# Performance work log

Measured on AMD Instinct MI355X. Metric: run time of the kernel, lower is better.

Reference implementation:

```python
import jax, jax.numpy as jnp
import numpy as np

V, BLOCK, D, H, LAYERS = 32000, 1024, 1024, 16, 4
KD = D // H  # key_dim = value_dim = head_size = 64
B, T = 4, 1024


def _ln(x, g, b, eps=1e-5):
    mu = jnp.mean(x, axis=-1, keepdims=True)
    var = jnp.mean((x - mu) ** 2, axis=-1, keepdims=True)
    return (x - mu) * jax.lax.rsqrt(var + eps) * g + b


def setup_inputs() -> dict:
    key = jax.random.key(0)
    ks = jax.random.split(key, 24)
    s = 0.02
    inp = {
        "x": jax.random.randint(ks[0], (B, T), 0, V),
        "tok_emb": jax.random.normal(ks[1], (V, D), jnp.float32) * s,
        "pos_emb": jax.random.normal(ks[2], (BLOCK, D), jnp.float32) * s,
        # per-head projections stacked over H (heads are identical since D % H == 0)
        "Wq": jax.random.normal(ks[3], (H, D, KD), jnp.float32) * s,
        "bq": jnp.zeros((H, KD), jnp.float32),
        "Wk": jax.random.normal(ks[4], (H, D, KD), jnp.float32) * s,
        "bk": jnp.zeros((H, KD), jnp.float32),
        "Wv": jax.random.normal(ks[5], (H, D, KD), jnp.float32) * s,
        "bv": jnp.zeros((H, KD), jnp.float32),
        "Wo": jax.random.normal(ks[6], (H, KD, KD), jnp.float32) * s,
        "bo": jnp.zeros((H, KD), jnp.float32),
        "W1": jax.random.normal(ks[7], (D, 4 * D), jnp.float32) * s,
        "b1": jnp.zeros((4 * D,), jnp.float32),
        "W2": jax.random.normal(ks[8], (4 * D, D), jnp.float32) * s,
        "b2": jnp.zeros((D,), jnp.float32),
        "ln1_g": jnp.ones((D,), jnp.float32),
        "ln1_b": jnp.zeros((D,), jnp.float32),
        "ln2_g": jnp.ones((D,), jnp.float32),
        "ln2_b": jnp.zeros((D,), jnp.float32),
        "lnf_g": jnp.ones((D,), jnp.float32),
        "lnf_b": jnp.zeros((D,), jnp.float32),
        "Wout": jax.random.normal(ks[9], (D, V), jnp.float32) * s,
        "bout": jnp.zeros((V,), jnp.float32),
    }
    return inp


def _forward(x, tok_emb, pos_emb, Wq, bq, Wk, bk, Wv, bv, Wo, bo,
             W1, b1, W2, b2, ln1_g, ln1_b, ln2_g, ln2_b, lnf_g, lnf_b, Wout, bout):
    h = tok_emb[x] + pos_emb[jnp.arange(x.shape[1])]  # [B,T,D]
    scale = 1.0 / np.sqrt(KD)
    # NOTE: [TransformerBlock()] * layers in the source ties ONE block's
    # weights across all layers, so the same params are applied LAYERS times.
    for _ in range(LAYERS):
        xn = _ln(h, ln1_g, ln1_b)
        q = jnp.einsum('btd,hdk->bhtk', xn, Wq) + bq[:, None, :]
        k = jnp.einsum('btd,hdk->bhtk', xn, Wk) + bk[:, None, :]
        v = jnp.einsum('btd,hdk->bhtk', xn, Wv) + bv[:, None, :]
        scores = jnp.einsum('bhtk,bhsk->bhts', q, k) * scale
        # source quirk: tril then `scores == 0 -> -inf` (also masks exact zeros)
        scores = jnp.tril(scores)
        scores = jnp.where(scores == 0.0, -jnp.inf, scores)
        wts = jax.nn.softmax(scores, axis=-1)
        y = jnp.einsum('bhts,bhsv->bhtv', wts, v)
        o = jnp.einsum('bhtv,hvo->bhto', y, Wo) + bo[:, None, :]
        attn = o.transpose(0, 2, 1, 3).reshape(h.shape)  # concat heads -> [B,T,D]
        h = h + attn
        xn2 = _ln(h, ln2_g, ln2_b)
        ff = jax.nn.relu(xn2 @ W1 + b1) @ W2 + b2
        h = h + ff
    return _ln(h, lnf_g, lnf_b) @ Wout + bout  # logits [B,T,V]


def reference(x, tok_emb, pos_emb, Wq, bq, Wk, bk, Wv, bv, Wo, bo,
              W1, b1, W2, b2, ln1_g, ln1_b, ln2_g, ln2_b, lnf_g, lnf_b, Wout, bout):
    return _forward(x, tok_emb, pos_emb, Wq, bq, Wk, bk, Wv, bv, Wo, bo,
                    W1, b1, W2, b2, ln1_g, ln1_b, ln2_g, ln2_b,
                    lnf_g, lnf_b, Wout, bout)
```

## Files before the change

kernel.cpp:

```cpp
#include <hip/hip_runtime.h>
#include <hip/hip_bf16.h>

typedef __hip_bfloat16 bf16;
typedef __attribute__((ext_vector_type(8))) short s16x8;
typedef __attribute__((ext_vector_type(4))) short s16x4;
typedef __attribute__((ext_vector_type(4))) float f32x4;

#define NEG_INF (-__builtin_inff())

union V8 { s16x8 v8; s16x4 v4[2]; };

__device__ inline s16x8 ldfrag(const bf16* p) {
    V8 f;
    f.v4[0] = *(const s16x4*)p;
    f.v4[1] = *(const s16x4*)(p + 4);
    return f.v8;
}

__device__ inline unsigned short f2bu(float f) {
    union { bf16 b; unsigned short u; } c;
    c.b = __float2bfloat16(f);
    return c.u;
}

__device__ inline float bu2f(unsigned short u) {
    union { bf16 b; unsigned short u; } c;
    c.u = u;
    return __bfloat162float(c.b);
}

__device__ inline void gload16(const bf16* gsrc, const bf16* ldst) {
    __builtin_amdgcn_global_load_lds(
        (const __attribute__((address_space(1))) unsigned int*)(unsigned long long)gsrc,
        (__attribute__((address_space(3))) unsigned int*)(unsigned int)(unsigned long long)ldst,
        16, 0, 0);
}

__global__ void sniff_kernel(const unsigned short* __restrict__ tok, int* __restrict__ flag)
{
    int big = 0;
    for (int i = threadIdx.x; i < 2048; i += 64) {
        unsigned e = (tok[i] >> 7) & 0xFFu;
        if (e >= 127u) big++;
    }
    #pragma unroll
    for (int off = 32; off; off >>= 1) big += __shfl_down(big, off);
    if (threadIdx.x == 0) *flag = (big > 64) ? 1 : 0;
}

__global__ __launch_bounds__(256) void transpose_cvt_kernel(
    const void* __restrict__ in, bf16* __restrict__ out,
    int N, int K, long in_bs, long out_bs, const int* __restrict__ flag)
{
    __shared__ float tile[32][33];
    const int f32 = *flag;
    const int z = blockIdx.z;
    const int n0 = blockIdx.x * 32, k0 = blockIdx.y * 32;
    const int r  = threadIdx.x >> 3;
    const int c4 = (threadIdx.x & 7) * 4;
    if (f32) {
        const float* ip = (const float*)in + z * in_bs;
        float4 v = *(const float4*)(ip + (long)(k0 + r) * N + n0 + c4);
        tile[r][c4 + 0] = v.x; tile[r][c4 + 1] = v.y;
        tile[r][c4 + 2] = v.z; tile[r][c4 + 3] = v.w;
    } else {
        const bf16* ip = (const bf16*)in + z * in_bs;
        ushort4 v = *(const ushort4*)(ip + (long)(k0 + r) * N + n0 + c4);
        tile[r][c4 + 0] = bu2f(v.x); tile[r][c4 + 1] = bu2f(v.y);
        tile[r][c4 + 2] = bu2f(v.z); tile[r][c4 + 3] = bu2f(v.w);
    }
    __syncthreads();
    bf16* op = out + z * out_bs;
    ushort4 o;
    o.x = f2bu(tile[c4 + 0][r]); o.y = f2bu(tile[c4 + 1][r]);
    o.z = f2bu(tile[c4 + 2][r]); o.w = f2bu(tile[c4 + 3][r]);
    *(ushort4*)(op + (long)(n0 + r) * K + k0 + c4) = o;
}

__global__ __launch_bounds__(256) void cvt_bias_kernel(
    const void* __restrict__ in, float* __restrict__ out, int n,
    const int* __restrict__ flag)
{
    int i = blockIdx.x * 256 + threadIdx.x;
    if (i < n)
        out[i] = (*flag) ? ((const float*)in)[i]
                         : __bfloat162float(((const bf16*)in)[i]);
}

__global__ __launch_bounds__(256) void embed_kernel(
    const int* __restrict__ x, const void* __restrict__ tok,
    const void* __restrict__ pos, float* __restrict__ h,
    const int* __restrict__ flag)
{
    const int f32 = *flag;
    int row = blockIdx.x;
    int t = row & 1023;
    int id = x[row];
    float* hp = h + (long)row * 1024;
    if (f32) {
        const float* tp = (const float*)tok + (long)id * 1024;
        const float* pp = (const float*)pos + (long)t * 1024;
        for (int c = threadIdx.x; c < 1024; c += 256)
            hp[c] = tp[c] + pp[c];
    } else {
        const bf16* tp = (const bf16*)tok + (long)id * 1024;
        const bf16* pp = (const bf16*)pos + (long)t * 1024;
        for (int c = threadIdx.x; c < 1024; c += 256)
            hp[c] = __bfloat162float(tp[c]) + __bfloat162float(pp[c]);
    }
}

__global__ __launch_bounds__(256) void ln_kernel(
    const float* __restrict__ h, const void* __restrict__ g,
    const void* __restrict__ b, bf16* __restrict__ out,
    const int* __restrict__ flag)
{
    __shared__ float red[8];
    const int f32 = *flag;
    int row = blockIdx.x;
    const float* hp = h + (long)row * 1024;
    int t = threadIdx.x;
    float4 xv = ((const float4*)hp)[t];
    float s  = xv.x + xv.y + xv.z + xv.w;
    float ss = xv.x*xv.x + xv.y*xv.y + xv.z*xv.z + xv.w*xv.w;
    #pragma unroll
    for (int off = 32; off; off >>= 1) {
        s  += __shfl_down(s, off);
        ss += __shfl_down(ss, off);
    }
    int wv = t >> 6, lane = t & 63;
    if (lane == 0) { red[wv] = s; red[4 + wv] = ss; }
    __syncthreads();
    float fs  = red[0] + red[1] + red[2] + red[3];
    float fss = red[4] + red[5] + red[6] + red[7];
    float mu  = fs * (1.0f / 1024.0f);
    float var = fss * (1.0f / 1024.0f) - mu * mu;
    float rstd = rsqrtf(fmaxf(var, 0.f) + 1e-5f);
    bf16* op = out + (long)row * 1024;
    #pragma unroll
    for (int i = 0; i < 4; i++) {
        int c = t * 4 + i;
        float gv, bv_;
        if (f32) { gv = ((const float*)g)[c]; bv_ = ((const float*)b)[c]; }
        else     { gv = __bfloat162float(((const bf16*)g)[c]); bv_ = __bfloat162float(((const bf16*)b)[c]); }
        float xn = (((const float*)&xv)[i] - mu) * rstd;
        op[c] = __float2bfloat16(xn * gv + bv_);
    }
}

template<bool RELU, bool RES_ADD, bool DYN_OUT>
__global__ __launch_bounds__(256) void gemm_kernel(
    const bf16* __restrict__ A, int lda, long a_bs,
    const void* __restrict__ B, int ldb, long b_bs,
    const void* __restrict__ bias, int bias_bs,
    void* __restrict__ Cv, int ldc, long c_bs, int K,
    const int* __restrict__ flag)
{
    __shared__ bf16 As[64][36];
    __shared__ bf16 Bs[64][36];
    const int f32 = *flag;
    const int tid = threadIdx.x;
    const int z = blockIdx.z;
    const bf16*  Ab   = A + (long)z * a_bs + (long)blockIdx.x * 64 * lda;
    const bf16*  Bb16 = (const bf16*)B  + (long)z * b_bs + (long)blockIdx.y * 64;
    const float* Bb32 = (const float*)B + (long)z * b_bs + (long)blockIdx.y * 64;
    const int wv = tid >> 6, lane = tid & 63, l16 = lane & 15, quad = lane >> 4;

    f32x4 acc[4];
    #pragma unroll
    for (int s = 0; s < 4; s++) { f32x4 z4 = {0.f,0.f,0.f,0.f}; acc[s] = z4; }

    const bool doA = tid < 128;
    const int ht = tid & 127;
    const int arow = ht >> 1;
    const int ak   = (ht & 1) * 16;
    const int bn   = (ht & 7) * 8;
    const int kp   = (ht >> 3) * 2;

    for (int k0 = 0; k0 < K; k0 += 32) {
        if (doA) {
            const bf16* src = Ab + (long)arow * lda + k0 + ak;
            V8 t0, t1;
            t0.v8 = *(const s16x8*)src;
            t1.v8 = *(const s16x8*)(src + 8);
            *(s16x4*)&As[arow][ak]      = t0.v4[0];
            *(s16x4*)&As[arow][ak + 4]  = t0.v4[1];
            *(s16x4*)&As[arow][ak + 8]  = t1.v4[0];
            *(s16x4*)&As[arow][ak + 12] = t1.v4[1];
        } else if (!f32) {
            const bf16* src = Bb16 + (long)(k0 + kp) * ldb + bn;
            s16x8 r0 = *(const s16x8*)src;
            s16x8 r1 = *(const s16x8*)(src + ldb);
            #pragma unroll
            for (int j = 0; j < 8; ++j) {
                unsigned int lo = (unsigned short)r0[j];
                unsigned int hi = (unsigned short)r1[j];
                *(unsigned int*)&Bs[bn + j][kp] = lo | (hi << 16);
            }
        } else {
            const float* src = Bb32 + (long)(k0 + kp) * ldb + bn;
            float4 a0 = *(const float4*)src;
            float4 a1 = *(const float4*)(src + 4);
            float4 c0 = *(const float4*)(src + ldb);
            float4 c1 = *(const float4*)(src + ldb + 4);
            float av[8] = {a0.x,a0.y,a0.z,a0.w,a1.x,a1.y,a1.z,a1.w};
            float cw[8] = {c0.x,c0.y,c0.z,c0.w,c1.x,c1.y,c1.z,c1.w};
            #pragma unroll
            for (int j = 0; j < 8; ++j) {
                unsigned int lo = f2bu(av[j]);
                unsigned int hi = f2bu(cw[j]);
                *(unsigned int*)&Bs[bn + j][kp] = lo | (hi << 16);
            }
        }
        __syncthreads();
        s16x8 af = ldfrag(&As[wv * 16 + l16][quad * 8]);
        #pragma unroll
        for (int s = 0; s < 4; ++s) {
            s16x8 bfr = ldfrag(&Bs[s * 16 + l16][quad * 8]);
            acc[s] = __builtin_amdgcn_mfma_f32_16x16x32_bf16(af, bfr, acc[s], 0, 0, 0);
        }
        __syncthreads();
    }

    const int gr0 = blockIdx.x * 64 + wv * 16 + quad * 4;
    const int gc0 = blockIdx.y * 64 + l16;
    #pragma unroll
    for (int s = 0; s < 4; ++s) {
        int gc = gc0 + s * 16;
        long bidx = (long)z * bias_bs + gc;
        float bv_ = f32 ? ((const float*)bias)[bidx]
                        : __bfloat162float(((const bf16*)bias)[bidx]);
        #pragma unroll
        for (int r = 0; r < 4; ++r) {
            long idx = (long)(gr0 + r) * ldc + gc;
            if (RES_ADD) {
                float* C = (float*)Cv + (long)z * c_bs;
                C[idx] += acc[s][r] + bv_;
            } else {
                float val = acc[s][r] + bv_;
                if (RELU) val = fmaxf(val, 0.f);
                if (DYN_OUT && f32)
                    ((float*)Cv)[(long)z * c_bs + idx] = val;
                else
                    ((bf16*)Cv)[(long)z * c_bs + idx] = __float2bfloat16(val);
            }
        }
    }
}

template<bool RELU, bool RES_ADD, bool DYN_OUT>
__global__ __launch_bounds__(256) void gemm_bt_kernel(
    const bf16* __restrict__ A, int lda,
    const bf16* __restrict__ Bt,
    const float* __restrict__ bias,
    void* __restrict__ Cv, int ldc, int K,
    const int* __restrict__ flag)
{
    __shared__ bf16 As[4096];
    __shared__ bf16 Bs[4096];
    const int tid = threadIdx.x;
    const int wv = tid >> 6, lane = tid & 63, l16 = lane & 15, quad = lane >> 4;
    const int wr = wv >> 1, wc = wv & 1;

    const int gx = gridDim.x;
    int nwg = gx * gridDim.y;
    int lin = blockIdx.y * gx + blockIdx.x;
    int cpx = nwg >> 3;
    int swz = (lin & 7) * cpx + (lin >> 3);
    const int m0 = (swz % gx) * 128;
    const int n0 = (swz / gx) * 128;

    const int srow = lane >> 2;
    const int scol = (lane & 3) * 8;

    const bf16* Ap  = A  + (long)(m0 + wv * 16 + srow) * lda + scol;
    const bf16* Ap2 = A  + (long)(m0 + 64 + wv * 16 + srow) * lda + scol;
    const bf16* Bp  = Bt + (long)(n0 + wv * 16 + srow) * K + scol;
    const bf16* Bp2 = Bt + (long)(n0 + 64 + wv * 16 + srow) * K + scol;
    const bf16* lA  = &As[wv * 512];
    const bf16* lA2 = &As[2048 + wv * 512];
    const bf16* lB  = &Bs[wv * 512];
    const bf16* lB2 = &Bs[2048 + wv * 512];

    f32x4 acc[4][4];
    #pragma unroll
    for (int i = 0; i < 4; ++i)
        #pragma unroll
        for (int j = 0; j < 4; ++j) { f32x4 z4 = {0.f,0.f,0.f,0.f}; acc[i][j] = z4; }

    for (int k0 = 0; k0 < K; k0 += 32) {
        gload16(Ap  + k0, lA);
        gload16(Ap2 + k0, lA2);
        gload16(Bp  + k0, lB);
        gload16(Bp2 + k0, lB2);
        __syncthreads();
        s16x8 af[4], bfv[4];
        #pragma unroll
        for (int i = 0; i < 4; ++i)
            af[i] = *(const s16x8*)&As[(wr * 64 + i * 16 + l16) * 32 + quad * 8];
        #pragma unroll
        for (int j = 0; j < 4; ++j)
            bfv[j] = *(const s16x8*)&Bs[(wc * 64 + j * 16 + l16) * 32 + quad * 8];
        #pragma unroll
        for (int i = 0; i < 4; ++i)
            #pragma unroll
            for (int j = 0; j < 4; ++j)
                acc[i][j] = __builtin_amdgcn_mfma_f32_16x16x32_bf16(af[i], bfv[j], acc[i][j], 0, 0, 0);
        __syncthreads();
    }

    const int f32o = DYN_OUT ? *flag : 0;
    #pragma unroll
    for (int j = 0; j < 4; ++j) {
        int col = n0 + wc * 64 + j * 16 + l16;
        float bv_ = bias[col];
        #pragma unroll
        for (int i = 0; i < 4; ++i) {
            int row = m0 + wr * 64 + i * 16 + quad * 4;
            #pragma unroll
            for (int r = 0; r < 4; ++r) {
                float val = acc[i][j][r] + bv_;
                long idx = (long)(row + r) * ldc + col;
                if (RES_ADD) {
                    ((float*)Cv)[idx] += val;
                } else if (DYN_OUT && f32o) {
                    ((float*)Cv)[idx] = val;
                } else {
                    if (RELU) val = fmaxf(val, 0.f);
                    ((bf16*)Cv)[idx] = __float2bfloat16(val);
                }
            }
        }
    }
}

__global__ __launch_bounds__(256) void flash_kernel(
    const bf16* __restrict__ qkv, bf16* __restrict__ y)
{
    __shared__ bf16 Qs[64][72];
    __shared__ bf16 Ks[64][72];
    __shared__ bf16 Vt[64][72];
    __shared__ bf16 Ps[4][16][72];

    const int tid = threadIdx.x;
    const int wv = tid >> 6, lane = tid & 63, l16 = lane & 15, quad = lane >> 4;
    const int h = blockIdx.z >> 2, b = blockIdx.z & 3;
    const bf16* qp = qkv + (long)b * 1024 * 3072 + h * 64;
    const bf16* kp = qp + 1024;
    const bf16* vp = qp + 2048;
    const int q0 = blockIdx.x * 64;

    {
        int row = tid >> 2, c0 = (tid & 3) * 16;
        const bf16* src = qp + (long)(q0 + row) * 3072 + c0;
        *(s16x8*)&Qs[row][c0]     = *(const s16x8*)src;
        *(s16x8*)&Qs[row][c0 + 8] = *(const s16x8*)(src + 8);
    }
    __syncthreads();
    s16x8 qa0 = *(const s16x8*)&Qs[wv * 16 + l16][quad * 8];
    s16x8 qa1 = *(const s16x8*)&Qs[wv * 16 + l16][32 + quad * 8];

    float m_i[4] = {NEG_INF, NEG_INF, NEG_INF, NEG_INF};
    float l_i[4] = {0.f, 0.f, 0.f, 0.f};
    f32x4 o[4];
    #pragma unroll
    for (int s = 0; s < 4; s++) { f32x4 z4 = {0.f,0.f,0.f,0.f}; o[s] = z4; }
    const int qrow_w = q0 + wv * 16 + quad * 4;

    const int nst = blockIdx.x + 1;
    for (int st = 0; st < nst; ++st) {
        const int s0 = st * 64;
        __syncthreads();
        {
            int row = tid >> 2, c0 = (tid & 3) * 16;
            const bf16* src = kp + (long)(s0 + row) * 3072 + c0;
            *(s16x8*)&Ks[row][c0]     = *(const s16x8*)src;
            *(s16x8*)&Ks[row][c0 + 8] = *(const s16x8*)(src + 8);
            int c0v = (tid & 7) * 8, sp = (tid >> 3) * 2;
            const bf16* vsrc = vp + (long)(s0 + sp) * 3072 + c0v;
            s16x8 vlo = *(const s16x8*)vsrc;
            s16x8 vhi = *(const s16x8*)(vsrc + 3072);
            #pragma unroll
            for (int j = 0; j < 8; ++j) {
                unsigned int lo = (unsigned short)vlo[j];
                unsigned int hi = (unsigned short)vhi[j];
                *(unsigned int*)&Vt[c0v + j][sp] = lo | (hi << 16);
            }
        }
        __syncthreads();

        f32x4 S[4];
        #pragma unroll
        for (int s = 0; s < 4; ++s) {
            f32x4 z4 = {0.f,0.f,0.f,0.f};
            s16x8 kb0 = *(const s16x8*)&Ks[s * 16 + l16][quad * 8];
            s16x8 kb1 = *(const s16x8*)&Ks[s * 16 + l16][32 + quad * 8];
            z4 = __builtin_amdgcn_mfma_f32_16x16x32_bf16(qa0, kb0, z4, 0, 0, 0);
            z4 = __builtin_amdgcn_mfma_f32_16x16x32_bf16(qa1, kb1, z4, 0, 0, 0);
            S[s] = z4;
        }
        #pragma unroll
        for (int s = 0; s < 4; ++s) {
            int sg = s0 + s * 16 + l16;
            #pragma unroll
            for (int r = 0; r < 4; ++r) {
                float val = S[s][r] * 0.125f;
                if (sg > qrow_w + r) val = NEG_INF;
                S[s][r] = val;
            }
        }
        float alpha[4];
        #pragma unroll
        for (int r = 0; r < 4; ++r) {
            float mx = fmaxf(fmaxf(S[0][r], S[1][r]), fmaxf(S[2][r], S[3][r]));
            #pragma unroll
            for (int off = 1; off < 16; off <<= 1)
                mx = fmaxf(mx, __shfl_xor(mx, off));
            float mnew = fmaxf(m_i[r], mx);
            alpha[r] = __expf(fmaxf(m_i[r] - mnew, -80.f));
            m_i[r] = mnew;
        }
        float rs[4] = {0.f, 0.f, 0.f, 0.f};
        #pragma unroll
        for (int s = 0; s < 4; ++s)
            #pragma unroll
            for (int r = 0; r < 4; ++r) {
                float p = __expf(fmaxf(S[s][r] - m_i[r], -80.f));
                S[s][r] = p;
                rs[r] += p;
            }
        #pragma unroll
        for (int r = 0; r < 4; ++r) {
            #pragma unroll
            for (int off = 1; off < 16; off <<= 1)
                rs[r] += __shfl_xor(rs[r], off);
            l_i[r] = l_i[r] * alpha[r] + rs[r];
        }
        #pragma unroll
        for (int s = 0; s < 4; ++s)
            #pragma unroll
            for (int r = 0; r < 4; ++r)
                Ps[wv][quad * 4 + r][s * 16 + l16] = __float2bfloat16(S[s][r]);
        __syncthreads();
        s16x8 pa0 = *(const s16x8*)&Ps[wv][l16][quad * 8];
        s16x8 pa1 = *(const s16x8*)&Ps[wv][l16][32 + quad * 8];
        #pragma unroll
        for (int s = 0; s < 4; ++s) {
            #pragma unroll
            for (int r = 0; r < 4; ++r) o[s][r] *= alpha[r];
            s16x8 vb0 = *(const s16x8*)&Vt[s * 16 + l16][quad * 8];
            s16x8 vb1 = *(const s16x8*)&Vt[s * 16 + l16][32 + quad * 8];
            o[s] = __builtin_amdgcn_mfma_f32_16x16x32_bf16(pa0, vb0, o[s], 0, 0, 0);
            o[s] = __builtin_amdgcn_mfma_f32_16x16x32_bf16(pa1, vb1, o[s], 0, 0, 0);
        }
    }
    float inv[4];
    #pragma unroll
    for (int r = 0; r < 4; ++r) inv[r] = 1.0f / l_i[r];
    bf16* yp = y + (long)b * 1024 * 1024 + h * 64;
    #pragma unroll
    for (int s = 0; s < 4; ++s)
        #pragma unroll
        for (int r = 0; r < 4; ++r)
            yp[(long)(qrow_w + r) * 1024 + s * 16 + l16] = __float2bfloat16(o[s][r] * inv[r]);
}

extern "C" void kernel_launch(void* const* d_in, const int* in_sizes, int n_in,
                              void* d_out, int out_size, void* d_ws, size_t ws_size,
                              hipStream_t stream)
{
    const int*  x    = (const int*)d_in[0];
    const void* tok  = d_in[1];
    const void* pos  = d_in[2];
    const void* Wq   = d_in[3];
    const void* bq   = d_in[4];
    const void* Wk   = d_in[5];
    const void* bk_  = d_in[6];
    const void* Wv   = d_in[7];
    const void* bv   = d_in[8];
    const void* Wo   = d_in[9];
    const void* bo   = d_in[10];
    const void* W1   = d_in[11];
    const void* b1   = d_in[12];
    const void* W2   = d_in[13];
    const void* b2   = d_in[14];
    const void* ln1g = d_in[15];
    const void* ln1b = d_in[16];
    const void* ln2g = d_in[17];
    const void* ln2b = d_in[18];
    const void* lnfg = d_in[19];
    const void* lnfb = d_in[20];
    const void* Wout = d_in[21];
    const void* bout = d_in[22];

    char* w = (char*)d_ws;
    int* flagp = (int*)w;        w += 256;
    float* h   = (float*)w;      w += 4096L * 1024 * 4;
    bf16* xn   = (bf16*)w;       w += 4096L * 1024 * 2;
    bf16* qkvb = (bf16*)w;       w += 4096L * 3072 * 2;
    bf16* yb   = (bf16*)w;       w += 4096L * 1024 * 2;
    bf16* mid  = (bf16*)w;       w += 4096L * 4096 * 2;
    bf16* WqkvT = (bf16*)w;      w += 3072L * 1024 * 2;
    bf16* W1T  = (bf16*)w;       w += 4096L * 1024 * 2;
    bf16* W2T  = (bf16*)w;       w += 1024L * 4096 * 2;
    bf16* WoutT = (bf16*)w;      w += 32000L * 1024 * 2;
    float* bqkvf = (float*)w;    w += 3072L * 4;
    float* b1f  = (float*)w;     w += 4096L * 4;
    float* b2f  = (float*)w;     w += 1024L * 4;
    float* boutf = (float*)w;    w += 32000L * 4;

    sniff_kernel<<<1, 64, 0, stream>>>((const unsigned short*)tok, flagp);

    transpose_cvt_kernel<<<dim3(2, 32, 16), 256, 0, stream>>>(
        Wq, WqkvT, 64, 1024, 65536, 65536, flagp);
    transpose_cvt_kernel<<<dim3(2, 32, 16), 256, 0, stream>>>(
        Wk, WqkvT + 1024L * 1024, 64, 1024, 65536, 65536, flagp);
    transpose_cvt_kernel<<<dim3(2, 32, 16), 256, 0, stream>>>(
        Wv, WqkvT + 2048L * 1024, 64, 1024, 65536, 65536, flagp);
    transpose_cvt_kernel<<<dim3(128, 32, 1), 256, 0, stream>>>(
        W1, W1T, 4096, 1024, 0, 0, flagp);
    transpose_cvt_kernel<<<dim3(32, 128, 1), 256, 0, stream>>>(
        W2, W2T, 1024, 4096, 0, 0, flagp);
    transpose_cvt_kernel<<<dim3(1000, 32, 1), 256, 0, stream>>>(
        Wout, WoutT, 32000, 1024, 0, 0, flagp);
    cvt_bias_kernel<<<4, 256, 0, stream>>>(bq, bqkvf, 1024, flagp);
    cvt_bias_kernel<<<4, 256, 0, stream>>>(bk_, bqkvf + 1024, 1024, flagp);
    cvt_bias_kernel<<<4, 256, 0, stream>>>(bv, bqkvf + 2048, 1024, flagp);
    cvt_bias_kernel<<<16, 256, 0, stream>>>(b1, b1f, 4096, flagp);
    cvt_bias_kernel<<<4, 256, 0, stream>>>(b2, b2f, 1024, flagp);
    cvt_bias_kernel<<<125, 256, 0, stream>>>(bout, boutf, 32000, flagp);

    embed_kernel<<<4096, 256, 0, stream>>>(x, tok, pos, h, flagp);

    for (int layer = 0; layer < 4; ++layer) {
        ln_kernel<<<4096, 256, 0, stream>>>(h, ln1g, ln1b, xn, flagp);
        gemm_bt_kernel<false,false,false><<<dim3(32, 24), 256, 0, stream>>>(
            xn, 1024, WqkvT, bqkvf, qkvb, 3072, 1024, flagp);
        flash_kernel<<<dim3(16, 1, 64), 256, 0, stream>>>(qkvb, yb);
        gemm_kernel<false,true,false><<<dim3(64, 1, 16), 256, 0, stream>>>(
            yb, 1024, 64, Wo, 64, 4096, bo, 64, h, 1024, 64, 64, flagp);
        ln_kernel<<<4096, 256, 0, stream>>>(h, ln2g, ln2b, xn, flagp);
        gemm_bt_kernel<true,false,false><<<dim3(32, 32), 256, 0, stream>>>(
            xn, 1024, W1T, b1f, mid, 4096, 1024, flagp);
        gemm_bt_kernel<false,true,false><<<dim3(32, 8), 256, 0, stream>>>(
            mid, 4096, W2T, b2f, h, 1024, 4096, flagp);
    }

    ln_kernel<<<4096, 256, 0, stream>>>(h, lnfg, lnfb, xn, flagp);
    gemm_bt_kernel<false,false,true><<<dim3(32, 250), 256, 0, stream>>>(
        xn, 1024, WoutT, boutf, d_out, 32000, 1024, flagp);
}
```

Measured before the change: 2.616 ms.

## Double-buffer GEMM LDS tiles, swizzle LDS, and run Wo as block-diagonal GEMM

The main GEMM kernel gets two LDS buffers so the next K-slice's global-to-LDS loads are issued while MFMAs run on the current slice, removing one barrier wait per step. An XOR swizzle on LDS columns is meant to reduce bank conflicts on fragment reads. The per-head Wo projection is expanded into a dense 1024x1024 block-diagonal transposed weight and run through the tuned GEMM. That replaces the small, poorly tiled batched kernel at the cost of 16x redundant zero FLOPs, and LDS use doubles, which may lower occupancy.

```diff
diff --git a/kernel.cpp b/kernel.cpp
--- a/kernel.cpp
+++ b/kernel.cpp
@@ -9,13 +9,6 @@
 #define NEG_INF (-__builtin_inff())
 
 union V8 { s16x8 v8; s16x4 v4[2]; };
-
-__device__ inline s16x8 ldfrag(const bf16* p) {
-    V8 f;
-    f.v4[0] = *(const s16x4*)p;
-    f.v4[1] = *(const s16x4*)(p + 4);
-    return f.v8;
-}
 
 __device__ inline unsigned short f2bu(float f) {
     union { bf16 b; unsigned short u; } c;
@@ -87,6 +80,22 @@
                          : __bfloat162float(((const bf16*)in)[i]);
 }
 
+__global__ __launch_bounds__(256) void prep_wo_kernel(
+    const void* __restrict__ Wo, bf16* __restrict__ WoT, const int* __restrict__ flag)
+{
+    const int f32 = *flag;
+    int idx = blockIdx.x * 256 + threadIdx.x;
+    int n = idx >> 10, k = idx & 1023;
+    int h = n >> 6, o = n & 63, h2 = k >> 6, v = k & 63;
+    float val = 0.f;
+    if (h == h2) {
+        long widx = ((long)h * 64 + v) * 64 + o;
+        val = f32 ? ((const float*)Wo)[widx]
+                  : __bfloat162float(((const bf16*)Wo)[widx]);
+    }
+    WoT[idx] = __float2bfloat16(val);
+}
+
 __global__ __launch_bounds__(256) void embed_kernel(
     const int* __restrict__ x, const void* __restrict__ tok,
     const void* __restrict__ pos, float* __restrict__ h,
@@ -148,104 +157,32 @@
     }
 }
 
-template<bool RELU, bool RES_ADD, bool DYN_OUT>
-__global__ __launch_bounds__(256) void gemm_kernel(
-    const bf16* __restrict__ A, int lda, long a_bs,
-    const void* __restrict__ B, int ldb, long b_bs,
-    const void* __restrict__ bias, int bias_bs,
-    void* __restrict__ Cv, int ldc, long c_bs, int K,
-    const int* __restrict__ flag)
-{
-    __shared__ bf16 As[64][36];
-    __shared__ bf16 Bs[64][36];
-    const int f32 = *flag;
-    const int tid = threadIdx.x;
-    const int z = blockIdx.z;
-    const bf16*  Ab   = A + (long)z * a_bs + (long)blockIdx.x * 64 * lda;
-    const bf16*  Bb16 = (const bf16*)B  + (long)z * b_bs + (long)blockIdx.y * 64;
-    const float* Bb32 = (const float*)B + (long)z * b_bs + (long)blockIdx.y * 64;
-    const int wv = tid >> 6, lane = tid & 63, l16 = lane & 15, quad = lane >> 4;
-
-    f32x4 acc[4];
-    #pragma unroll
-    for (int s = 0; s < 4; s++) { f32x4 z4 = {0.f,0.f,0.f,0.f}; acc[s] = z4; }
-
-    const bool doA = tid < 128;
-    const int ht = tid & 127;
-    const int arow = ht >> 1;
-    const int ak   = (ht & 1) * 16;
-    const int bn   = (ht & 7) * 8;
-    const int kp   = (ht >> 3) * 2;
-
-    for (int k0 = 0; k0 < K; k0 += 32) {
-        if (doA) {
-            const bf16* src = Ab + (long)arow * lda + k0 + ak;
-            V8 t0, t1;
-            t0.v8 = *(const s16x8*)src;
-            t1.v8 = *(const s16x8*)(src + 8);
-            *(s16x4*)&As[arow][ak]      = t0.v4[0];
-            *(s16x4*)&As[arow][ak + 4]  = t0.v4[1];
-            *(s16x4*)&As[arow][ak + 8]  = t1.v4[0];
-            *(s16x4*)&As[arow][ak + 12] = t1.v4[1];
-        } else if (!f32) {
-            const bf16* src = Bb16 + (long)(k0 + kp) * ldb + bn;
-            s16x8 r0 = *(const s16x8*)src;
-            s16x8 r1 = *(const s16x8*)(src + ldb);
-            #pragma unroll
-            for (int j = 0; j < 8; ++j) {
-                unsigned int lo = (unsigned short)r0[j];
-                unsigned int hi = (unsigned short)r1[j];
-                *(unsigned int*)&Bs[bn + j][kp] = lo | (hi << 16);
-            }
-        } else {
-            const float* src = Bb32 + (long)(k0 + kp) * ldb + bn;
-            float4 a0 = *(const float4*)src;
-            float4 a1 = *(const float4*)(src + 4);
-            float4 c0 = *(const float4*)(src + ldb);
-            float4 c1 = *(const float4*)(src + ldb + 4);
-            float av[8] = {a0.x,a0.y,a0.z,a0.w,a1.x,a1.y,a1.z,a1.w};
-            float cw[8] = {c0.x,c0.y,c0.z,c0.w,c1.x,c1.y,c1.z,c1.w};
-            #pragma unroll
-            for (int j = 0; j < 8; ++j) {
-                unsigned int lo = f2bu(av[j]);
-                unsigned int hi = f2bu(cw[j]);
-                *(unsigned int*)&Bs[bn + j][kp] = lo | (hi << 16);
-            }
-        }
-        __syncthreads();
-        s16x8 af = ldfrag(&As[wv * 16 + l16][quad * 8]);
-        #pragma unroll
-        for (int s = 0; s < 4; ++s) {
-            s16x8 bfr = ldfrag(&Bs[s * 16 + l16][quad * 8]);
-            acc[s] = __builtin_amdgcn_mfma_f32_16x16x32_bf16(af, bfr, acc[s], 0, 0, 0);
-        }
-        __syncthreads();
-    }
-
-    const int gr0 = blockIdx.x * 64 + wv * 16 + quad * 4;
-    const int gc0 = blockIdx.y * 64 + l16;
-    #pragma unroll
-    for (int s = 0; s < 4; ++s) {
-        int gc = gc0 + s * 16;
-        long bidx = (long)z * bias_bs + gc;
-        float bv_ = f32 ? ((const float*)bias)[bidx]
-                        : __bfloat162float(((const bf16*)bias)[bidx]);
-        #pragma unroll
-        for (int r = 0; r < 4; ++r) {
-            long idx = (long)(gr0 + r) * ldc + gc;
-            if (RES_ADD) {
-                float* C = (float*)Cv + (long)z * c_bs;
-                C[idx] += acc[s][r] + bv_;
-            } else {
-                float val = acc[s][r] + bv_;
-                if (RELU) val = fmaxf(val, 0.f);
-                if (DYN_OUT && f32)
-                    ((float*)Cv)[(long)z * c_bs + idx] = val;
-                else
-                    ((bf16*)Cv)[(long)z * c_bs + idx] = __float2bfloat16(val);
-            }
-        }
-    }
+__device__ __forceinline__ void gemm_stage(
+    const bf16* Ap, const bf16* Ap2, const bf16* Bp, const bf16* Bp2,
+    bf16* asb, bf16* bsb, int wv, int koff)
+{
+    gload16(Ap + koff,  asb + wv * 512);
+    gload16(Ap2 + koff, asb + 2048 + wv * 512);
+    gload16(Bp + koff,  bsb + wv * 512);
+    gload16(Bp2 + koff, bsb + 2048 + wv * 512);
+}
+
+__device__ __forceinline__ void gemm_compute(
+    const bf16* __restrict__ asb, const bf16* __restrict__ bsb,
+    int wr, int wc, int l16, int rchunk, f32x4 (&acc)[4][4])
+{
+    s16x8 af[4], bfv[4];
+    #pragma unroll
+    for (int i = 0; i < 4; ++i)
+        af[i] = *(const s16x8*)&asb[(wr * 64 + i * 16 + l16) * 32 + rchunk];
+    #pragma unroll
+    for (int j = 0; j < 4; ++j)
+        bfv[j] = *(const s16x8*)&bsb[(wc * 64 + j * 16 + l16) * 32 + rchunk];
+    #pragma unroll
+    for (int i = 0; i < 4; ++i)
+        #pragma unroll
+        for (int j = 0; j < 4; ++j)
+            acc[i][j] = __builtin_amdgcn_mfma_f32_16x16x32_bf16(af[i], bfv[j], acc[i][j], 0, 0, 0);
 }
 
 template<bool RELU, bool RES_ADD, bool DYN_OUT>
@@ -256,8 +193,8 @@
     void* __restrict__ Cv, int ldc, int K,
     const int* __restrict__ flag)
 {
-    __shared__ bf16 As[4096];
-    __shared__ bf16 Bs[4096];
+    __shared__ bf16 As[2][4096];
+    __shared__ bf16 Bs[2][4096];
     const int tid = threadIdx.x;
     const int wv = tid >> 6, lane = tid & 63, l16 = lane & 15, quad = lane >> 4;
     const int wr = wv >> 1, wc = wv & 1;
@@ -271,16 +208,13 @@
     const int n0 = (swz / gx) * 128;
 
     const int srow = lane >> 2;
-    const int scol = (lane & 3) * 8;
+    const int scol = ((lane & 3) ^ ((lane >> 3) & 3)) * 8;
+    const int rchunk = (quad ^ ((l16 >> 1) & 3)) * 8;
 
     const bf16* Ap  = A  + (long)(m0 + wv * 16 + srow) * lda + scol;
     const bf16* Ap2 = A  + (long)(m0 + 64 + wv * 16 + srow) * lda + scol;
     const bf16* Bp  = Bt + (long)(n0 + wv * 16 + srow) * K + scol;
     const bf16* Bp2 = Bt + (long)(n0 + 64 + wv * 16 + srow) * K + scol;
-    const bf16* lA  = &As[wv * 512];
-    const bf16* lA2 = &As[2048 + wv * 512];
-    const bf16* lB  = &Bs[wv * 512];
-    const bf16* lB2 = &Bs[2048 + wv * 512];
 
     f32x4 acc[4][4];
     #pragma unroll
@@ -288,24 +222,17 @@
         #pragma unroll
         for (int j = 0; j < 4; ++j) { f32x4 z4 = {0.f,0.f,0.f,0.f}; acc[i][j] = z4; }
 
-    for (int k0 = 0; k0 < K; k0 += 32) {
-        gload16(Ap  + k0, lA);
-        gload16(Ap2 + k0, lA2);
-        gload16(Bp  + k0, lB);
-        gload16(Bp2 + k0, lB2);
+    gemm_stage(Ap, Ap2, Bp, Bp2, As[0], Bs[0], wv, 0);
+    __syncthreads();
+
+    for (int k0 = 0; k0 < K; k0 += 64) {
+        if (k0 + 32 < K)
+            gemm_stage(Ap, Ap2, Bp, Bp2, As[1], Bs[1], wv, k0 + 32);
+        gemm_compute(As[0], Bs[0], wr, wc, l16, rchunk, acc);
         __syncthreads();
-        s16x8 af[4], bfv[4];
-        #pragma unroll
-        for (int i = 0; i < 4; ++i)
-            af[i] = *(const s16x8*)&As[(wr * 64 + i * 16 + l16) * 32 + quad * 8];
-        #pragma unroll
-        for (int j = 0; j < 4; ++j)
-            bfv[j] = *(const s16x8*)&Bs[(wc * 64 + j * 16 + l16) * 32 + quad * 8];
-        #pragma unroll
-        for (int i = 0; i < 4; ++i)
-            #pragma unroll
-            for (int j = 0; j < 4; ++j)
-                acc[i][j] = __builtin_amdgcn_mfma_f32_16x16x32_bf16(af[i], bfv[j], acc[i][j], 0, 0, 0);
+        if (k0 + 64 < K)
+            gemm_stage(Ap, Ap2, Bp, Bp2, As[0], Bs[0], wv, k0 + 64);
+        gemm_compute(As[1], Bs[1], wr, wc, l16, rchunk, acc);
         __syncthreads();
     }
 
@@ -504,9 +431,11 @@
     bf16* W1T  = (bf16*)w;       w += 4096L * 1024 * 2;
     bf16* W2T  = (bf16*)w;       w += 1024L * 4096 * 2;
     bf16* WoutT = (bf16*)w;      w += 32000L * 1024 * 2;
+    bf16* WoT  = (bf16*)w;       w += 1024L * 1024 * 2;
     float* bqkvf = (float*)w;    w += 3072L * 4;
     float* b1f  = (float*)w;     w += 4096L * 4;
     float* b2f  = (float*)w;     w += 1024L * 4;
+    float* bof  = (float*)w;     w += 1024L * 4;
     float* boutf = (float*)w;    w += 32000L * 4;
 
     sniff_kernel<<<1, 64, 0, stream>>>((const unsigned short*)tok, flagp);
@@ -523,11 +452,13 @@
         W2, W2T, 1024, 4096, 0, 0, flagp);
     transpose_cvt_kernel<<<dim3(1000, 32, 1), 256, 0, stream>>>(
         Wout, WoutT, 32000, 1024, 0, 0, flagp);
+    prep_wo_kernel<<<4096, 256, 0, stream>>>(Wo, WoT, flagp);
     cvt_bias_kernel<<<4, 256, 0, stream>>>(bq, bqkvf, 1024, flagp);
     cvt_bias_kernel<<<4, 256, 0, stream>>>(bk_, bqkvf + 1024, 1024, flagp);
     cvt_bias_kernel<<<4, 256, 0, stream>>>(bv, bqkvf + 2048, 1024, flagp);
     cvt_bias_kernel<<<16, 256, 0, stream>>>(b1, b1f, 4096, flagp);
     cvt_bias_kernel<<<4, 256, 0, stream>>>(b2, b2f, 1024, flagp);
+    cvt_bias_kernel<<<4, 256, 0, stream>>>(bo, bof, 1024, flagp);
     cvt_bias_kernel<<<125, 256, 0, stream>>>(bout, boutf, 32000, flagp);
 
     embed_kernel<<<4096, 256, 0, stream>>>(x, tok, pos, h, flagp);
@@ -537,8 +468,8 @@
         gemm_bt_kernel<false,false,false><<<dim3(32, 24), 256, 0, stream>>>(
             xn, 1024, WqkvT, bqkvf, qkvb, 3072, 1024, flagp);
         flash_kernel<<<dim3(16, 1, 64), 256, 0, stream>>>(qkvb, yb);
-        gemm_kernel<false,true,false><<<dim3(64, 1, 16), 256, 0, stream>>>(
-            yb, 1024, 64, Wo, 64, 4096, bo, 64, h, 1024, 64, 64, flagp);
+        gemm_bt_kernel<false,true,false><<<dim3(32, 8), 256, 0, stream>>>(
+            yb, 1024, WoT, bof, h, 1024, 1024, flagp);
         ln_kernel<<<4096, 256, 0, stream>>>(h, ln2g, ln2b, xn, flagp);
         gemm_bt_kernel<true,false,false><<<dim3(32, 32), 256, 0, stream>>>(
             xn, 1024, W1T, b1f, mid, 4096, 1024, flagp);
```

After: 2.424 ms. 7.3% less time.
